# Kernel optimization log

Hardware: AMD Instinct MI355X
Metric: run time of the kernel (lower is better)

The kernel has to match this reference:

```python
import jax, jax.numpy as jnp
import numpy as np

H = 16          # num_attention_heads
DH = 64         # attention_head_size
HID = H * DH    # hidden_size = 1024
EPS = 1e-12


def _layernorm(x, gamma, beta):
    mu = jnp.mean(x, axis=-1, keepdims=True)
    var = jnp.mean(jnp.square(x - mu), axis=-1, keepdims=True)
    return (x - mu) * jax.lax.rsqrt(var + EPS) * gamma + beta


def _attention(q, k, v, mask, Wo, bo, gamma, beta):
    # q,k,v: [B,S,HID] already linearly projected
    B, Tq, _ = q.shape
    Tk = k.shape[1]
    qh = q.reshape(B, Tq, H, DH)
    kh = k.reshape(B, Tk, H, DH)
    vh = v.reshape(B, Tk, H, DH)
    scores = jnp.einsum('bqhd,bkhd->bhqk', qh, kh) / np.sqrt(DH).astype(q.dtype)
    if mask is not None:
        scores = scores + mask  # mask broadcasts [B,1,1,Tk]
    probs = jax.nn.softmax(scores, axis=-1)
    ctx = jnp.einsum('bhqk,bkhd->bqhd', probs, vh)
    proj = jnp.einsum('bqhd,hdo->bqo', ctx, Wo) + bo
    # NOTE: residual is the projected query q (faithful to the source)
    return _layernorm(q + proj, gamma, beta)


def setup_inputs() -> dict:
    key = jax.random.key(0)
    ks = jax.random.split(key, 20)
    B, T, S = 4, 1024, 1024
    s = 0.02
    inp = {
        'encoder_states': jax.random.normal(ks[0], (B, S, HID), jnp.float32),
        'decoder_inputs': jax.random.normal(ks[1], (B, T, HID), jnp.float32),
        'src_attention_mask': jnp.zeros((B, 1, 1, S), jnp.float32),
        'tgt_attention_mask': jnp.zeros((B, 1, 1, T), jnp.float32),
        'Wq': jax.random.normal(ks[2], (HID, HID), jnp.float32) * s,
        'bq': jnp.zeros((HID,), jnp.float32),
        'Wk': jax.random.normal(ks[3], (HID, HID), jnp.float32) * s,
        'bk': jnp.zeros((HID,), jnp.float32),
        'Wv': jax.random.normal(ks[4], (HID, HID), jnp.float32) * s,
        'bv': jnp.zeros((HID,), jnp.float32),
        'Wq2': jax.random.normal(ks[5], (HID, HID), jnp.float32) * s,
        'bq2': jnp.zeros((HID,), jnp.float32),
        'Wk2': jax.random.normal(ks[6], (HID, HID), jnp.float32) * s,
        'bk2': jnp.zeros((HID,), jnp.float32),
        'Wv2': jax.random.normal(ks[7], (HID, HID), jnp.float32) * s,
        'bv2': jnp.zeros((HID,), jnp.float32),
        'Wo': jax.random.normal(ks[8], (H, DH, HID), jnp.float32) * s,
        'bo': jnp.zeros((HID,), jnp.float32),
        'gamma': jnp.ones((HID,), jnp.float32),
        'beta': jnp.zeros((HID,), jnp.float32),
    }
    return inp


def reference(encoder_states, decoder_inputs, src_attention_mask, tgt_attention_mask,
              Wq, bq, Wk, bk, Wv, bv, Wq2, bq2, Wk2, bk2, Wv2, bv2,
              Wo, bo, gamma, beta):
    # self-attention over decoder inputs
    q1 = decoder_inputs @ Wq + bq
    k1 = decoder_inputs @ Wk + bk
    v1 = decoder_inputs @ Wv + bv
    self_out = _attention(q1, k1, v1, tgt_attention_mask, Wo, bo, gamma, beta)
    # cross-attention: query from self_out, key/value from encoder states
    q2 = self_out @ Wq2 + bq2
    k2 = encoder_states @ Wk2 + bk2
    v2 = encoder_states @ Wv2 + bv2
    return _attention(q2, k2, v2, src_attention_mask, Wo, bo, gamma, beta)
```

## Files before the change

### kernel.cpp

```cpp
#include <hip/hip_runtime.h>
#include <stdint.h>


typedef unsigned short u16;
typedef __bf16 bf16x8 __attribute__((ext_vector_type(8)));
typedef float f32x4 __attribute__((ext_vector_type(4)));

#define AS1 __attribute__((address_space(1)))
#define AS3 __attribute__((address_space(3)))
typedef AS3 char lds_char;
typedef AS3 unsigned short lds_u16;

#define VMCNT(n) asm volatile("s_waitcnt vmcnt(" #n ")" ::: "memory")
#define LGKM0() asm volatile("s_waitcnt lgkmcnt(0)" ::: "memory")
#define SBARRIER() asm volatile("s_barrier" ::: "memory")

__device__ __forceinline__ u16 f2bf(float f) {
  union { float f; uint32_t u; } v; v.f = f;
  uint32_t u = v.u;
  return (u16)((u + 0x7fffu + ((u >> 16) & 1u)) >> 16);
}

__device__ __forceinline__ float bf2f(u16 b) {
  union { uint32_t u; float f; } v; v.u = ((uint32_t)b) << 16;
  return v.f;
}

__device__ __forceinline__ uint32_t cvt_pk_bf16(float lo, float hi) {
  uint32_t r;
  asm("v_cvt_pk_bf16_f32 %0, %1, %2" : "=v"(r) : "v"(lo), "v"(hi));
  return r;
}

__device__ __forceinline__ void gl_lds16(const void* g, void* l) {
  __builtin_amdgcn_global_load_lds((AS1 void*)(g), (AS3 void*)(l), 16, 0, 0);
}

__device__ __forceinline__ bf16x8 dsr128(const lds_u16* p) {
  bf16x8 r;
  asm volatile("ds_read_b128 %0, %1" : "=v"(r) : "v"(p));
  return r;
}

__device__ __forceinline__ int swz(int row, int byte) {
  return row * 128 + (byte ^ ((row & 7) << 4));
}

__global__ void __launch_bounds__(256)
convert2_kernel(const float* __restrict__ in0, u16* __restrict__ out0,
                const float* __restrict__ in1, u16* __restrict__ out1) {
  const int half = blockIdx.x >> 12;
  const int i = (blockIdx.x & 4095) * 256 + threadIdx.x;
  const float* in = half ? in1 : in0;
  u16* out = half ? out1 : out0;
  float4 v = ((const float4*)in)[i];
  ushort4 o;
  o.x = f2bf(v.x); o.y = f2bf(v.y); o.z = f2bf(v.z); o.w = f2bf(v.w);
  ((ushort4*)out)[i] = o;
}

struct WP { const float* w[7]; };

__global__ void __launch_bounds__(256)
transpose_kernel(WP wp, u16* __restrict__ out) {
  __shared__ float tile[64][65];
  const float* W = wp.w[blockIdx.z];
  u16* Wt = out + (size_t)blockIdx.z * 1024 * 1024;
  const int k0 = blockIdx.y * 64, n0 = blockIdx.x * 64;
  const int t = threadIdx.x;
  const int r = t >> 4, c4 = (t & 15) * 4;
#pragma unroll
  for (int rr = 0; rr < 64; rr += 16) {
    float4 v = *(const float4*)&W[(size_t)(k0 + r + rr) * 1024 + n0 + c4];
    tile[r + rr][c4 + 0] = v.x; tile[r + rr][c4 + 1] = v.y;
    tile[r + rr][c4 + 2] = v.z; tile[r + rr][c4 + 3] = v.w;
  }
  __syncthreads();
  const int n = t >> 2, seg = (t & 3) * 16;
  union { u16 s[16]; uint4 q[2]; } u;
#pragma unroll
  for (int i = 0; i < 16; ++i) u.s[i] = f2bf(tile[seg + i][n]);
  uint4* dst = (uint4*)&Wt[(size_t)(n0 + n) * 1024 + k0 + seg];
  dst[0] = u.q[0]; dst[1] = u.q[1];
}

__global__ void __launch_bounds__(512, 2)
qkv4b_kernel(const u16* __restrict__ A0, const u16* __restrict__ A1,
             const u16* __restrict__ A2, const u16* __restrict__ Bt,
             const float* __restrict__ b0, const float* __restrict__ b1,
             const float* __restrict__ b2,
             u16* __restrict__ qb, u16* __restrict__ kb, u16* __restrict__ vt) {
  __shared__ u16 Alds[4][256 * 32];
  __shared__ u16 Blds[4][256 * 32];

  const int d = blockIdx.y * 12 + blockIdx.x;
  const int c = d & 7, ci = d >> 3;
  const int mt = (c & 3) * 4 + (ci & 3);
  const int nt = (c >> 2) * 6 + (ci >> 2);
  const int bm = mt * 256, bn = nt * 256;
  const int seg = nt >> 2;
  const u16* A = (seg == 0) ? A0 : (seg == 1) ? A1 : A2;

  const int t = threadIdx.x, wv = t >> 6, ln = t & 63;
  const int wm = (wv >> 2) * 128, wn = (wv & 3) * 64;
  const int lcol = ln & 15, g = ln >> 4, lr4 = g * 4;
  const int aoff = (g * 16) ^ ((lcol & 3) << 4);

  lds_char* ABase = (lds_char*)&Alds[0][0];
  lds_char* BBase = (lds_char*)&Blds[0][0];

  const int st_row = wv * 16 + (ln >> 2);
  const int st_srcb = (((ln & 3) ^ ((ln >> 2) & 3)) * 16);
  auto stageA = [&](int buf, int k0) {
#pragma unroll
    for (int hf = 0; hf < 2; ++hf) {
      const int row = hf * 128 + st_row;
      gl_lds16((const char*)A + ((size_t)(bm + row) * 1024 + k0) * 2 + st_srcb,
               (char*)ABase + buf * 16384 + hf * 8192 + wv * 1024);
    }
  };
  auto stageB = [&](int buf, int k0) {
#pragma unroll
    for (int hf = 0; hf < 2; ++hf) {
      const int row = hf * 128 + st_row;
      gl_lds16((const char*)Bt + ((size_t)(bn + row) * 1024 + k0) * 2 + st_srcb,
               (char*)BBase + buf * 16384 + hf * 8192 + wv * 1024);
    }
  };

  f32x4 acc[8][4] = {};

  stageA(0, 0); stageB(0, 0);
  stageA(1, 32); stageB(1, 32);
  VMCNT(4);
  __builtin_amdgcn_s_barrier();

  for (int kt = 0; kt < 32; ++kt) {
    const int buf = kt & 3;
    lds_char* Ab = ABase + buf * 16384;
    lds_char* Bb = BBase + buf * 16384;
    const int sbuf = (kt + 2) & 3;
    const int sk = (kt + 2) * 32;
    const bool do_st = kt < 30;
    bf16x8 afr[4], bfr[4];

#pragma unroll
    for (int j = 0; j < 4; ++j)
      bfr[j] = dsr128((const lds_u16*)(Bb + (wn + j * 16 + lcol) * 64 + aoff));
#pragma unroll
    for (int i = 0; i < 4; ++i)
      afr[i] = dsr128((const lds_u16*)(Ab + (wm + i * 16 + lcol) * 64 + aoff));
    if (do_st) stageA(sbuf, sk);
    __builtin_amdgcn_s_barrier();
    LGKM0();
    __builtin_amdgcn_sched_barrier(0);
    __builtin_amdgcn_s_setprio(1);
#pragma unroll
    for (int i = 0; i < 4; ++i)
#pragma unroll
      for (int j = 0; j < 4; ++j)
        acc[i][j] = __builtin_amdgcn_mfma_f32_16x16x32_bf16(afr[i], bfr[j], acc[i][j], 0, 0, 0);
    __builtin_amdgcn_s_setprio(0);
    __builtin_amdgcn_s_barrier();

#pragma unroll
    for (int i = 0; i < 4; ++i)
      afr[i] = dsr128((const lds_u16*)(Ab + (wm + 64 + i * 16 + lcol) * 64 + aoff));
    if (do_st) stageB(sbuf, sk);
    __builtin_amdgcn_s_barrier();
    LGKM0();
    __builtin_amdgcn_sched_barrier(0);
    __builtin_amdgcn_s_setprio(1);
#pragma unroll
    for (int i = 0; i < 4; ++i)
#pragma unroll
      for (int j = 0; j < 4; ++j)
        acc[4 + i][j] = __builtin_amdgcn_mfma_f32_16x16x32_bf16(afr[i], bfr[j], acc[4 + i][j], 0, 0, 0);
    __builtin_amdgcn_s_setprio(0);
    if (kt < 30) { VMCNT(4); }
    else if (kt == 30) { VMCNT(0); }
    __builtin_amdgcn_s_barrier();
  }

  const int cs = bn & 1023;
  const float* bias = (seg == 0) ? b0 : (seg == 1) ? b1 : b2;
  u16* outp = (seg == 0) ? qb : kb;
#pragma unroll
  for (int j = 0; j < 4; ++j) {
    const int col = cs + wn + j * 16 + lcol;
    const float bc = bias[col];
#pragma unroll
    for (int i = 0; i < 8; ++i) {
      const int row0 = bm + wm + i * 16 + lr4;
      if (seg == 2) {
        ushort4 o;
        o.x = f2bf(acc[i][j][0] + bc); o.y = f2bf(acc[i][j][1] + bc);
        o.z = f2bf(acc[i][j][2] + bc); o.w = f2bf(acc[i][j][3] + bc);
        const int b_ = row0 >> 10, s = row0 & 1023;
        const int h = col >> 6, dd = col & 63;
        *(ushort4*)&vt[(((size_t)(b_ * 16 + h) * 64 + dd) << 10) + s] = o;
      } else {
#pragma unroll
        for (int r = 0; r < 4; ++r)
          outp[(size_t)(row0 + r) * 1024 + col] = f2bf(acc[i][j][r] + bc);
      }
    }
  }
}

__global__ void __launch_bounds__(256)
gemm_proj(const u16* __restrict__ A, const u16* __restrict__ Bt,
          const float* __restrict__ bias, const u16* __restrict__ resid,
          float* __restrict__ outf) {
  __shared__ u16 Alds[2][8192];
  __shared__ u16 Blds[2][8192];
  const int d = blockIdx.y * 8 + blockIdx.x;
  const int c = d & 7, ci = d >> 3;
  const int mt = (c & 3) * 8 + (ci & 7);
  const int nt = (c >> 2) * 4 + (ci >> 3);
  const int bm = mt * 128, bn = nt * 128;
  const int t = threadIdx.x, wv = t >> 6, ln = t & 63;
  const int wm = (wv >> 1) * 64, wn = (wv & 1) * 64;
  const int lcol = ln & 15, lk8 = (ln >> 4) * 8, lr4 = (ln >> 4) * 4;

  f32x4 acc[4][4] = {};

  auto STAGE = [&](int buf, int k0) {
#pragma unroll
    for (int cc = 0; cc < 4; ++cc) {
      const int o = cc * 4096 + wv * 1024 + ln * 16;
      const int row = o >> 7, colb = o & 127;
      gl_lds16((const char*)A + ((size_t)(bm + row) * 1024 + k0) * 2 + colb,
               (char*)Alds[buf] + cc * 4096 + wv * 1024);
      gl_lds16((const char*)Bt + ((size_t)(bn + row) * 1024 + k0) * 2 + colb,
               (char*)Blds[buf] + cc * 4096 + wv * 1024);
    }
  };

  auto COMPUTE = [&](int buf) {
    const u16* Ab = Alds[buf];
    const u16* Bb = Blds[buf];
#pragma unroll
    for (int ks = 0; ks < 2; ++ks) {
      bf16x8 a[4], b[4];
#pragma unroll
      for (int i = 0; i < 4; ++i)
        a[i] = *(const bf16x8*)&Ab[(wm + i * 16 + lcol) * 64 + ks * 32 + lk8];
#pragma unroll
      for (int j = 0; j < 4; ++j)
        b[j] = *(const bf16x8*)&Bb[(wn + j * 16 + lcol) * 64 + ks * 32 + lk8];
#pragma unroll
      for (int i = 0; i < 4; ++i)
#pragma unroll
        for (int j = 0; j < 4; ++j)
          acc[i][j] = __builtin_amdgcn_mfma_f32_16x16x32_bf16(a[i], b[j], acc[i][j], 0, 0, 0);
    }
  };

  STAGE(0, 0);
  int cur = 0;
  for (int it = 0; it < 15; ++it) {
    STAGE(cur ^ 1, (it + 1) * 64);
    VMCNT(8);
    SBARRIER();
    COMPUTE(cur);
    SBARRIER();
    cur ^= 1;
  }
  VMCNT(0);
  SBARRIER();
  COMPUTE(cur);

#pragma unroll
  for (int j = 0; j < 4; ++j) {
    const int col = bn + wn + j * 16 + lcol;
    const float bc = bias[col];
#pragma unroll
    for (int i = 0; i < 4; ++i) {
      const int row0 = bm + wm + i * 16 + lr4;
#pragma unroll
      for (int r = 0; r < 4; ++r) {
        const size_t idx = (size_t)(row0 + r) * 1024 + col;
        outf[idx] = acc[i][j][r] + bc + bf2f(resid[idx]);
      }
    }
  }
}

__global__ void __launch_bounds__(256)
attn_kernel(const u16* __restrict__ Q, const u16* __restrict__ Kb,
            const u16* __restrict__ Vt, const float* __restrict__ mask,
            u16* __restrict__ ctx) {
  __shared__ u16 Klds[2][64 * 64];
  __shared__ u16 Vlds[2][64 * 64];
  __shared__ u16 Plds[4][16 * 64];

  const int fid = blockIdx.x;
  const int xcd = fid & 7, idx = fid >> 3;
  const int bh = xcd * 8 + (idx >> 4);
  const int b = bh >> 4, h = bh & 15;
  const int q0 = (idx & 15) * 64;

  const int t = threadIdx.x, wv = t >> 6, ln = t & 63;
  const int lcol = ln & 15, g = ln >> 4;
  const int lk8 = g * 8, c0 = g * 16;

  const int qrow = q0 + wv * 16 + lcol;
  const u16* qptr = Q + ((size_t)(b * 1024 + qrow) * 1024 + h * 64);
  bf16x8 qa[2];
  qa[0] = *(const bf16x8*)(qptr + lk8);
  qa[1] = *(const bf16x8*)(qptr + 32 + lk8);

  const float* mrow = mask + b * 1024;
  char* pbase = (char*)&Plds[wv][0];

  f32x4 accO[4] = {};
  float m_r = -1e30f, l_r = 0.f;

  auto STAGE = [&](int buf, int s0) {
#pragma unroll
    for (int c = 0; c < 2; ++c) {
      const int o = c * 4096 + wv * 1024 + ln * 16;
      const int row = o >> 7;
      const int src_cb = (o & 127) ^ ((row & 7) << 4);
      gl_lds16((const char*)Kb + ((size_t)((b * 1024 + s0 + row) * 1024 + h * 64)) * 2 + src_cb,
               (char*)Klds[buf] + c * 4096 + wv * 1024);
      gl_lds16((const char*)Vt + ((size_t)(((b * 16 + h) * 64 + row) * 1024 + s0)) * 2 + src_cb,
               (char*)Vlds[buf] + c * 4096 + wv * 1024);
    }
  };

  auto TILE = [&](int buf, const float4* mk) {
    f32x4 accST[4] = {};
    __builtin_amdgcn_s_setprio(1);
#pragma unroll
    for (int ks = 0; ks < 2; ++ks)
#pragma unroll
      for (int sb = 0; sb < 4; ++sb) {
        bf16x8 kb = *(const bf16x8*)((const char*)Klds[buf] + swz(sb * 16 + lcol, ks * 64 + c0));
        accST[sb] = __builtin_amdgcn_mfma_f32_16x16x32_bf16(kb, qa[ks], accST[sb], 0, 0, 0);
      }
    __builtin_amdgcn_s_setprio(0);

    float sv[4][4];
#pragma unroll
    for (int sb = 0; sb < 4; ++sb) {
      sv[sb][0] = accST[sb][0] * 0.125f + mk[sb].x;
      sv[sb][1] = accST[sb][1] * 0.125f + mk[sb].y;
      sv[sb][2] = accST[sb][2] * 0.125f + mk[sb].z;
      sv[sb][3] = accST[sb][3] * 0.125f + mk[sb].w;
    }
    float mt = sv[0][0];
#pragma unroll
    for (int sb = 0; sb < 4; ++sb)
#pragma unroll
      for (int r = 0; r < 4; ++r) mt = fmaxf(mt, sv[sb][r]);
    mt = fmaxf(mt, __shfl_xor(mt, 16));
    mt = fmaxf(mt, __shfl_xor(mt, 32));

    const bool nr = __all(mt <= m_r + 8.0f) != 0;
    float alpha = 1.0f;
    if (!nr) {
      const float mn2 = fmaxf(m_r, mt);
      alpha = __expf(m_r - mn2);
      m_r = mn2;
    }
    float rs = 0.f;
#pragma unroll
    for (int sb = 0; sb < 4; ++sb)
#pragma unroll
      for (int r = 0; r < 4; ++r) {
        const float pp = __expf(sv[sb][r] - m_r);
        sv[sb][r] = pp;
        rs += pp;
      }
    rs += __shfl_xor(rs, 16);
    rs += __shfl_xor(rs, 32);
    l_r = nr ? (l_r + rs) : (l_r * alpha + rs);

#pragma unroll
    for (int sb = 0; sb < 4; ++sb) {
      uint2 dd;
      dd.x = cvt_pk_bf16(sv[sb][0], sv[sb][1]);
      dd.y = cvt_pk_bf16(sv[sb][2], sv[sb][3]);
      *(uint2*)(pbase + swz(lcol, sb * 32 + g * 8)) = dd;
    }

    if (!nr) {
#pragma unroll
      for (int df = 0; df < 4; ++df)
#pragma unroll
        for (int r = 0; r < 4; ++r) accO[df][r] *= alpha;
    }
    __builtin_amdgcn_s_setprio(1);
#pragma unroll
    for (int ks = 0; ks < 2; ++ks) {
      bf16x8 pb = *(const bf16x8*)(pbase + swz(lcol, ks * 64 + c0));
#pragma unroll
      for (int df = 0; df < 4; ++df) {
        bf16x8 va = *(const bf16x8*)((const char*)Vlds[buf] + swz(df * 16 + lcol, ks * 64 + c0));
        accO[df] = __builtin_amdgcn_mfma_f32_16x16x32_bf16(va, pb, accO[df], 0, 0, 0);
      }
    }
    __builtin_amdgcn_s_setprio(0);
  };

  STAGE(0, 0);
  float4 mk_cur[4];
#pragma unroll
  for (int sb = 0; sb < 4; ++sb)
    mk_cur[sb] = *(const float4*)&mrow[sb * 16 + g * 4];

  int cur = 0;
  for (int ti = 0; ti < 15; ++ti) {
    const int s1 = ti * 64 + 64;
    STAGE(cur ^ 1, s1);
    float4 mk_nxt[4];
#pragma unroll
    for (int sb = 0; sb < 4; ++sb)
      mk_nxt[sb] = *(const float4*)&mrow[s1 + sb * 16 + g * 4];
    VMCNT(12);
    SBARRIER();
    TILE(cur, mk_cur);
    SBARRIER();
#pragma unroll
    for (int sb = 0; sb < 4; ++sb) mk_cur[sb] = mk_nxt[sb];
    cur ^= 1;
  }
  VMCNT(4);
  SBARRIER();
  TILE(cur, mk_cur);

  const float inv = 1.0f / l_r;
  u16* cp = ctx + ((size_t)(b * 1024 + qrow) * 1024 + h * 64);
#pragma unroll
  for (int df = 0; df < 4; ++df) {
    ushort4 o;
    o.x = f2bf(accO[df][0] * inv); o.y = f2bf(accO[df][1] * inv);
    o.z = f2bf(accO[df][2] * inv); o.w = f2bf(accO[df][3] * inv);
    *(ushort4*)(cp + df * 16 + g * 4) = o;
  }
}

template <int OUTF>
__global__ void __launch_bounds__(256)
ln_kernel(const float* __restrict__ x, const float* __restrict__ gamma,
          const float* __restrict__ beta, float* __restrict__ outf,
          u16* __restrict__ outb) {
  const int row = blockIdx.x, t = threadIdx.x;
  const float* xr = x + (size_t)row * 1024;
  float4 v = *(const float4*)&xr[t * 4];
  float s = v.x + v.y + v.z + v.w;
  float q = v.x * v.x + v.y * v.y + v.z * v.z + v.w * v.w;
#pragma unroll
  for (int off = 1; off < 64; off <<= 1) {
    s += __shfl_xor(s, off);
    q += __shfl_xor(q, off);
  }
  __shared__ float ws[4], wq[4];
  if ((t & 63) == 0) { ws[t >> 6] = s; wq[t >> 6] = q; }
  __syncthreads();
  s = ws[0] + ws[1] + ws[2] + ws[3];
  q = wq[0] + wq[1] + wq[2] + wq[3];
  const float mu = s * (1.0f / 1024.0f);
  float var = q * (1.0f / 1024.0f) - mu * mu;
  var = fmaxf(var, 0.0f);
  const float rstd = rsqrtf(var + 1e-12f);
  float4 g = *(const float4*)&gamma[t * 4];
  float4 be = *(const float4*)&beta[t * 4];
  float y0 = (v.x - mu) * rstd * g.x + be.x;
  float y1 = (v.y - mu) * rstd * g.y + be.y;
  float y2 = (v.z - mu) * rstd * g.z + be.z;
  float y3 = (v.w - mu) * rstd * g.w + be.w;
  if constexpr (OUTF) {
    float4 o; o.x = y0; o.y = y1; o.z = y2; o.w = y3;
    *(float4*)&outf[(size_t)row * 1024 + t * 4] = o;
  } else {
    ushort4 o; o.x = f2bf(y0); o.y = f2bf(y1); o.z = f2bf(y2); o.w = f2bf(y3);
    *(ushort4*)&outb[(size_t)row * 1024 + t * 4] = o;
  }
}

extern "C" void kernel_launch(void* const* d_in, const int* in_sizes, int n_in,
                              void* d_out, int out_size, void* d_ws, size_t ws_size,
                              hipStream_t stream) {
  const float* enc = (const float*)d_in[0];
  const float* dec = (const float*)d_in[1];
  const float* src_mask = (const float*)d_in[2];
  const float* tgt_mask = (const float*)d_in[3];
  const float* Wq  = (const float*)d_in[4];  const float* bq  = (const float*)d_in[5];
  const float* Wk  = (const float*)d_in[6];  const float* bk  = (const float*)d_in[7];
  const float* Wv  = (const float*)d_in[8];  const float* bv  = (const float*)d_in[9];
  const float* Wq2 = (const float*)d_in[10]; const float* bq2 = (const float*)d_in[11];
  const float* Wk2 = (const float*)d_in[12]; const float* bk2 = (const float*)d_in[13];
  const float* Wv2 = (const float*)d_in[14]; const float* bv2 = (const float*)d_in[15];
  const float* Wo  = (const float*)d_in[16]; const float* bo  = (const float*)d_in[17];
  const float* gamma = (const float*)d_in[18]; const float* beta = (const float*)d_in[19];
  float* out = (float*)d_out;

  char* p = (char*)d_ws;
  const size_t ABF = (size_t)4096 * 1024 * 2;
  const size_t AF  = (size_t)4096 * 1024 * 4;
  const size_t WBF = (size_t)1024 * 1024 * 2;
  u16* decbf = (u16*)p; p += ABF;
  u16* encbf = (u16*)p; p += ABF;
  u16* wt    = (u16*)p; p += 7 * WBF;
  u16* qbf   = (u16*)p; p += ABF;
  u16* kbf   = (u16*)p; p += ABF;
  u16* vtb   = (u16*)p; p += ABF;
  u16* ctxb  = (u16*)p; p += ABF;
  float* tmpf = (float*)p; p += AF;
  u16* sobf  = decbf;

  u16* WoT  = wt + 6 * 1048576;

  dim3 b256(256);
  convert2_kernel<<<8192, b256, 0, stream>>>(dec, decbf, enc, encbf);
  WP wp;
  wp.w[0] = Wq; wp.w[1] = Wk; wp.w[2] = Wv; wp.w[3] = Wq2;
  wp.w[4] = Wk2; wp.w[5] = Wv2; wp.w[6] = Wo;
  transpose_kernel<<<dim3(16, 16, 7), b256, 0, stream>>>(wp, wt);

  qkv4b_kernel<<<dim3(12, 16), 512, 0, stream>>>(
      decbf, decbf, decbf, wt, bq, bk, bv, qbf, kbf, vtb);
  attn_kernel<<<1024, b256, 0, stream>>>(qbf, kbf, vtb, tgt_mask, ctxb);
  gemm_proj<<<dim3(8, 32), b256, 0, stream>>>(ctxb, WoT, bo, qbf, tmpf);
  ln_kernel<0><<<4096, b256, 0, stream>>>(tmpf, gamma, beta, nullptr, sobf);
  qkv4b_kernel<<<dim3(12, 16), 512, 0, stream>>>(
      sobf, encbf, encbf, wt + 3 * 1048576, bq2, bk2, bv2, qbf, kbf, vtb);
  attn_kernel<<<1024, b256, 0, stream>>>(qbf, kbf, vtb, src_mask, ctxb);
  gemm_proj<<<dim3(8, 32), b256, 0, stream>>>(ctxb, WoT, bo, qbf, tmpf);
  ln_kernel<1><<<4096, b256, 0, stream>>>(tmpf, gamma, beta, out, nullptr);
}
```

Baseline: 234.2 us.

## Deepen QKV GEMM prefetch to three stages and stage epilogue through LDS

The QKV GEMM now prefetches three k-tiles ahead instead of two within its four LDS buffers, with wait counts adjusted to match, to hide more global-load latency. The LDS swizzle is changed to a different XOR pattern. The epilogue writes bias-added bf16 results into the shared buffer, then emits wide 16-byte coalesced global stores for both row-major Q/K and the transposed V layout, replacing scattered 2-byte and 8-byte stores. It reuses all 128KB of shared memory, which may limit occupancy to one block per CU, and adds a barrier before the store phase.

Result: no change. 233.9 us (-0.1%).

```diff
diff --git a/kernel.cpp b/kernel.cpp
--- a/kernel.cpp
+++ b/kernel.cpp
@@ -85,13 +85,12 @@
 }
 
 __global__ void __launch_bounds__(512, 2)
-qkv4b_kernel(const u16* __restrict__ A0, const u16* __restrict__ A1,
+qkv4c_kernel(const u16* __restrict__ A0, const u16* __restrict__ A1,
              const u16* __restrict__ A2, const u16* __restrict__ Bt,
              const float* __restrict__ b0, const float* __restrict__ b1,
              const float* __restrict__ b2,
              u16* __restrict__ qb, u16* __restrict__ kb, u16* __restrict__ vt) {
-  __shared__ u16 Alds[4][256 * 32];
-  __shared__ u16 Blds[4][256 * 32];
+  __shared__ u16 SH[65536];
 
   const int d = blockIdx.y * 12 + blockIdx.x;
   const int c = d & 7, ci = d >> 3;
@@ -103,20 +102,20 @@
 
   const int t = threadIdx.x, wv = t >> 6, ln = t & 63;
   const int wm = (wv >> 2) * 128, wn = (wv & 3) * 64;
-  const int lcol = ln & 15, g = ln >> 4, lr4 = g * 4;
-  const int aoff = (g * 16) ^ ((lcol & 3) << 4);
-
-  lds_char* ABase = (lds_char*)&Alds[0][0];
-  lds_char* BBase = (lds_char*)&Blds[0][0];
+  const int lcol = ln & 15, g = ln >> 4;
+  const int aoff = (g * 16) ^ (((lcol >> 1) & 3) << 4);
+
+  lds_char* ABase = (lds_char*)&SH[0];
+  lds_char* BBase = (lds_char*)&SH[32768];
 
   const int st_row = wv * 16 + (ln >> 2);
-  const int st_srcb = (((ln & 3) ^ ((ln >> 2) & 3)) * 16);
+  const int st_srcb = (((ln & 3) ^ ((ln >> 3) & 3)) * 16);
   auto stageA = [&](int buf, int k0) {
 #pragma unroll
     for (int hf = 0; hf < 2; ++hf) {
       const int row = hf * 128 + st_row;
       gl_lds16((const char*)A + ((size_t)(bm + row) * 1024 + k0) * 2 + st_srcb,
-               (char*)ABase + buf * 16384 + hf * 8192 + wv * 1024);
+               (char*)&SH[0] + buf * 16384 + hf * 8192 + wv * 1024);
     }
   };
   auto stageB = [&](int buf, int k0) {
@@ -124,7 +123,7 @@
     for (int hf = 0; hf < 2; ++hf) {
       const int row = hf * 128 + st_row;
       gl_lds16((const char*)Bt + ((size_t)(bn + row) * 1024 + k0) * 2 + st_srcb,
-               (char*)BBase + buf * 16384 + hf * 8192 + wv * 1024);
+               (char*)&SH[32768] + buf * 16384 + hf * 8192 + wv * 1024);
     }
   };
 
@@ -132,16 +131,17 @@
 
   stageA(0, 0); stageB(0, 0);
   stageA(1, 32); stageB(1, 32);
-  VMCNT(4);
+  stageA(2, 64); stageB(2, 64);
+  VMCNT(8);
   __builtin_amdgcn_s_barrier();
 
   for (int kt = 0; kt < 32; ++kt) {
     const int buf = kt & 3;
     lds_char* Ab = ABase + buf * 16384;
     lds_char* Bb = BBase + buf * 16384;
-    const int sbuf = (kt + 2) & 3;
-    const int sk = (kt + 2) * 32;
-    const bool do_st = kt < 30;
+    const int sbuf = (kt + 3) & 3;
+    const int sk = (kt + 3) * 32;
+    const bool do_st = kt < 29;
     bf16x8 afr[4], bfr[4];
 
 #pragma unroll
@@ -177,33 +177,60 @@
       for (int j = 0; j < 4; ++j)
         acc[4 + i][j] = __builtin_amdgcn_mfma_f32_16x16x32_bf16(afr[i], bfr[j], acc[4 + i][j], 0, 0, 0);
     __builtin_amdgcn_s_setprio(0);
-    if (kt < 30) { VMCNT(4); }
+    if (kt < 29)       { VMCNT(8); }
+    else if (kt == 29) { VMCNT(4); }
     else if (kt == 30) { VMCNT(0); }
     __builtin_amdgcn_s_barrier();
   }
 
   const int cs = bn & 1023;
   const float* bias = (seg == 0) ? b0 : (seg == 1) ? b1 : b2;
-  u16* outp = (seg == 0) ? qb : kb;
-#pragma unroll
-  for (int j = 0; j < 4; ++j) {
-    const int col = cs + wn + j * 16 + lcol;
-    const float bc = bias[col];
-#pragma unroll
-    for (int i = 0; i < 8; ++i) {
-      const int row0 = bm + wm + i * 16 + lr4;
-      if (seg == 2) {
+
+  if (seg == 2) {
+#pragma unroll
+    for (int j = 0; j < 4; ++j) {
+      const int col_l = wn + j * 16 + lcol;
+      const float bc = bias[cs + col_l];
+#pragma unroll
+      for (int i = 0; i < 8; ++i) {
+        const int m4 = wm + i * 16 + g * 4;
         ushort4 o;
         o.x = f2bf(acc[i][j][0] + bc); o.y = f2bf(acc[i][j][1] + bc);
         o.z = f2bf(acc[i][j][2] + bc); o.w = f2bf(acc[i][j][3] + bc);
-        const int b_ = row0 >> 10, s = row0 & 1023;
-        const int h = col >> 6, dd = col & 63;
-        *(ushort4*)&vt[(((size_t)(b_ * 16 + h) * 64 + dd) << 10) + s] = o;
-      } else {
+        *(ushort4*)((char*)SH + col_l * 512 + ((m4 * 2) ^ ((col_l & 7) << 4))) = o;
+      }
+    }
+  } else {
+#pragma unroll
+    for (int j = 0; j < 4; ++j) {
+      const int col_l = wn + j * 16 + lcol;
+      const float bc = bias[cs + col_l];
+#pragma unroll
+      for (int i = 0; i < 8; ++i) {
+        const int m0 = wm + i * 16 + g * 4;
 #pragma unroll
         for (int r = 0; r < 4; ++r)
-          outp[(size_t)(row0 + r) * 1024 + col] = f2bf(acc[i][j][r] + bc);
+          SH[(m0 + r) * 256 + (col_l ^ (((m0 + r) & 7) << 3))] = f2bf(acc[i][j][r] + bc);
       }
+    }
+  }
+  __builtin_amdgcn_s_barrier();
+
+  {
+    const int R = t >> 1, hb = t & 1;
+    u16* gp;
+    if (seg == 2) {
+      const int col = cs + R;
+      const int h = col >> 6, dd = col & 63;
+      gp = vt + ((size_t)((bm >> 10) * 16 + h) * 64 + dd) * 1024 + (bm & 1023) + hb * 128;
+    } else {
+      u16* outp = (seg == 0) ? qb : kb;
+      gp = outp + (size_t)(bm + R) * 1024 + cs + hb * 128;
+    }
+#pragma unroll
+    for (int cix = 0; cix < 16; ++cix) {
+      uint4 v = *(uint4*)((char*)SH + R * 512 + ((hb * 256 + cix * 16) ^ ((R & 7) << 4)));
+      *(uint4*)(gp + cix * 8) = v;
     }
   }
 }
@@ -521,12 +548,12 @@
   wp.w[4] = Wk2; wp.w[5] = Wv2; wp.w[6] = Wo;
   transpose_kernel<<<dim3(16, 16, 7), b256, 0, stream>>>(wp, wt);
 
-  qkv4b_kernel<<<dim3(12, 16), 512, 0, stream>>>(
+  qkv4c_kernel<<<dim3(12, 16), 512, 0, stream>>>(
       decbf, decbf, decbf, wt, bq, bk, bv, qbf, kbf, vtb);
   attn_kernel<<<1024, b256, 0, stream>>>(qbf, kbf, vtb, tgt_mask, ctxb);
   gemm_proj<<<dim3(8, 32), b256, 0, stream>>>(ctxb, WoT, bo, qbf, tmpf);
   ln_kernel<0><<<4096, b256, 0, stream>>>(tmpf, gamma, beta, nullptr, sobf);
-  qkv4b_kernel<<<dim3(12, 16), 512, 0, stream>>>(
+  qkv4c_kernel<<<dim3(12, 16), 512, 0, stream>>>(
       sobf, encbf, encbf, wt + 3 * 1048576, bq2, bk2, bv2, qbf, kbf, vtb);
   attn_kernel<<<1024, b256, 0, stream>>>(qbf, kbf, vtb, src_mask, ctxb);
   gemm_proj<<<dim3(8, 32), b256, 0, stream>>>(ctxb, WoT, bo, qbf, tmpf);
```
